# Kernel tuning notes

Measured on AMD Instinct MI355X. Metric: run time of the kernel, lower is better.

The kernel has to match this reference:

```python
import jax, jax.numpy as jnp
import numpy as np

B, C, H, W = 16, 256, 64, 64
DQ = C // 4


def setup_inputs() -> dict:
    key = jax.random.key(0)
    ks = jax.random.split(key, 6)
    scale = 1.0 / np.sqrt(C)
    return {
        "x_query": jax.random.normal(ks[0], (B, C, W, H), jnp.float32),
        "x_key": jax.random.normal(ks[1], (B, C, W, H), jnp.float32),
        "x_value": jax.random.normal(ks[2], (B, C, W, H), jnp.float32),
        "Wq": jax.random.normal(ks[3], (DQ, C), jnp.float32) * scale,
        "bq": jnp.zeros((DQ,), jnp.float32),
        "Wk": jax.random.normal(ks[4], (DQ, C), jnp.float32) * scale,
        "bk": jnp.zeros((DQ,), jnp.float32),
        "Wv": jax.random.normal(ks[5], (C, C), jnp.float32) * scale,
        "bv": jnp.zeros((C,), jnp.float32),
    }


def reference(x_query, x_key, x_value, Wq, bq, Wk, bk, Wv, bv):
    b, c, w, h = x_value.shape
    n = w * h
    # 1x1 convs == per-pixel linear over channels; flatten spatial to n
    q = (jnp.einsum('oc,bcn->bon', Wq, x_query.reshape(b, c, n))
         + bq[None, :, None])            # [b, dq, n]
    k = (jnp.einsum('oc,bcn->bon', Wk, x_key.reshape(b, c, n))
         + bk[None, :, None])            # [b, dq, n]
    v = (jnp.einsum('oc,bcn->bon', Wv, x_value.reshape(b, c, n))
         + bv[None, :, None])            # [b, c, n]
    # energy = Q^T K  (unscaled), softmax over last dim
    energy = jnp.einsum('bdi,bdj->bij', q, k)        # [b, n, n]
    attention = jax.nn.softmax(energy, axis=-1)
    # out = V @ attention : out[b,c,i] = sum_j V[b,c,j] * att[b,j,i]
    out = jnp.einsum('bcj,bji->bci', v, attention)   # [b, c, n]
    return out.reshape(b, c, w, h)
```

## Files before the change

### kernel.cpp

```cpp
#include <hip/hip_runtime.h>
#include <hip/hip_bf16.h>
#include <stddef.h>

#define BATCH 16
#define CH    256
#define NPIX  4096
#define DQH   64
#define L2E   1.44269504088896340736f

typedef __attribute__((ext_vector_type(8))) short bf16x8;
typedef __attribute__((ext_vector_type(4))) float floatx4;

__device__ __forceinline__ unsigned short f2bf(float f) {
  union { float f; unsigned int u; } v; v.f = f;
  unsigned int u = v.u;
  u += 0x7fffu + ((u >> 16) & 1u);
  return (unsigned short)(u >> 16);
}

__device__ __forceinline__ unsigned int pk2bf(float a, float b) {
  __hip_bfloat162 h = __float22bfloat162_rn(float2{a, b});
  union { __hip_bfloat162 h; unsigned int u; } cv;
  cv.h = h;
  return cv.u;
}

__device__ __forceinline__ bf16x8 ldbf8(const unsigned short* p) {
  return *(const bf16x8*)p;
}

__device__ __forceinline__ int xcd_swz(int lin, int nwg) {
  return (lin & 7) * (nwg >> 3) + (lin >> 3);
}

__device__ __forceinline__ void gload_lds16(const void* g, void* l) {
  __builtin_amdgcn_global_load_lds(
      (const __attribute__((address_space(1))) void*)g,
      (__attribute__((address_space(3))) void*)l, 16, 0, 0);
}

__global__ __launch_bounds__(256) void wconv_kernel(
    const float* __restrict__ Wq, const float* __restrict__ Wk,
    const float* __restrict__ Wv, unsigned short* __restrict__ Wb) {
  const int idx = blockIdx.x * 256 + threadIdx.x;
  float v;
  if (idx < 64 * CH)            v = Wq[idx] * L2E;
  else if (idx < 128 * CH)      v = Wk[idx - 64 * CH];
  else                          v = Wv[idx - 128 * CH];
  Wb[idx] = f2bf(v);
}

__global__ __launch_bounds__(256) void proj_kernel(
    const float* __restrict__ xq, const float* __restrict__ xk,
    const float* __restrict__ xv, const unsigned short* __restrict__ Wb,
    const float* __restrict__ bq, const float* __restrict__ bk,
    const float* __restrict__ bv,
    unsigned short* __restrict__ Qb, unsigned short* __restrict__ Kb,
    unsigned short* __restrict__ Vb) {
  __shared__ __attribute__((aligned(16))) float xtile[32][256];
  const int t    = threadIdx.x;
  const int lane = t & 63;
  const int w    = t >> 6;
  const int l15  = lane & 15;
  const int quad = lane >> 4;
  const int b    = blockIdx.y;
  const int pxbase = blockIdx.x * 256;
  const int z    = blockIdx.z;

  const float* X; const float* bt; int dbase; int wbase;
  if (z == 0)      { X = xq; bt = bq; dbase = 0;            wbase = 0; }
  else if (z == 1) { X = xk; bt = bk; dbase = 0;            wbase = 64; }
  else             { X = xv; bt = bv; dbase = (z - 2) * 64; wbase = 128 + (z - 2) * 64; }

  floatx4 acc[4][4];
#pragma unroll
  for (int mt = 0; mt < 4; ++mt)
#pragma unroll
    for (int nt = 0; nt < 4; ++nt)
      acc[mt][nt] = (floatx4){0.f, 0.f, 0.f, 0.f};

  const float* xb0 = X + (size_t)b * CH * NPIX + pxbase;

  for (int kb = 0; kb < 8; ++kb) {
#pragma unroll
    for (int i = 0; i < 8; ++i) {
      const int cloc = w + i * 4;
      const int rot  = (cloc >> 3) << 3;
      const int colf = ((lane << 2) - rot) & 255;
      gload_lds16(xb0 + (size_t)(kb * 32 + cloc) * NPIX + colf,
                  &xtile[cloc][0]);
    }
    __syncthreads();

#pragma unroll
    for (int nt = 0; nt < 4; ++nt) {
      const int pxl = w * 64 + nt * 16 + l15;
      float f[8];
#pragma unroll
      for (int j = 0; j < 8; ++j) {
        const int row = quad * 8 + j;
        f[j] = xtile[row][(pxl + ((row >> 3) << 3)) & 255];
      }
      union { bf16x8 v; unsigned int u[4]; } bb;
      bb.u[0] = pk2bf(f[0], f[1]);
      bb.u[1] = pk2bf(f[2], f[3]);
      bb.u[2] = pk2bf(f[4], f[5]);
      bb.u[3] = pk2bf(f[6], f[7]);
#pragma unroll
      for (int mt = 0; mt < 4; ++mt) {
        const bf16x8 aA =
            ldbf8(Wb + (size_t)(wbase + mt * 16 + l15) * CH + kb * 32 + quad * 8);
        acc[mt][nt] =
            __builtin_amdgcn_mfma_f32_16x16x32_bf16(aA, bb.v, acc[mt][nt], 0, 0, 0);
      }
    }
    __syncthreads();
  }

  float4 bias4[4];
#pragma unroll
  for (int mt = 0; mt < 4; ++mt)
    bias4[mt] = *(const float4*)&bt[dbase + mt * 16 + quad * 4];
  if (z == 0) {
#pragma unroll
    for (int mt = 0; mt < 4; ++mt) {
      bias4[mt].x *= L2E; bias4[mt].y *= L2E;
      bias4[mt].z *= L2E; bias4[mt].w *= L2E;
    }
  }

  if (z >= 2) {
#pragma unroll
    for (int mt = 0; mt < 4; ++mt)
#pragma unroll
      for (int nt = 0; nt < 4; ++nt) {
        const int px = pxbase + w * 64 + nt * 16 + l15;
#pragma unroll
        for (int r = 0; r < 4; ++r) {
          const int c = dbase + mt * 16 + quad * 4 + r;
          Vb[((size_t)b * CH + c) * NPIX + px] =
              f2bf(acc[mt][nt][r] + ((const float*)&bias4[mt])[r]);
        }
      }
  } else {
    unsigned short* Ob = (z == 0) ? Qb : Kb;
#pragma unroll
    for (int mt = 0; mt < 4; ++mt)
#pragma unroll
      for (int nt = 0; nt < 4; ++nt) {
        const int px = pxbase + w * 64 + nt * 16 + l15;
        uint2 qp;
        qp.x = pk2bf(acc[mt][nt][0] + ((const float*)&bias4[mt])[0],
                     acc[mt][nt][1] + ((const float*)&bias4[mt])[1]);
        qp.y = pk2bf(acc[mt][nt][2] + ((const float*)&bias4[mt])[2],
                     acc[mt][nt][3] + ((const float*)&bias4[mt])[3]);
        *(uint2*)&Ob[((size_t)b * NPIX + px) * DQH + mt * 16 + quad * 4] = qp;
      }
  }
}

__global__ __launch_bounds__(256) void pass1_kernel(
    const unsigned short* __restrict__ Qb, const unsigned short* __restrict__ Kb,
    float* __restrict__ Srow) {
  const int t    = threadIdx.x;
  const int lane = t & 63;
  const int w    = t >> 6;
  const int l15  = lane & 15;
  const int quad = lane >> 4;
  const int lin  = blockIdx.x + (blockIdx.y << 6);
  const int swz  = xcd_swz(lin, 64 * BATCH);
  const int b     = swz >> 6;
  const int jbase = (swz & 63) * 64 + w * 16;

  const unsigned short* qrow = Qb + ((size_t)b * NPIX + jbase + l15) * DQH;
  const bf16x8 qA0 = ldbf8(qrow + quad * 8);
  const bf16x8 qA1 = ldbf8(qrow + 32 + quad * 8);

  float lsum[4] = {0.f, 0.f, 0.f, 0.f};

  const unsigned short* kbase = Kb + (size_t)b * NPIX * DQH;

  bf16x8 kC[4][2], kN[4][2];
#pragma unroll
  for (int nt = 0; nt < 4; ++nt) {
    const unsigned short* krow = kbase + (size_t)(nt * 16 + l15) * DQH;
    kC[nt][0] = ldbf8(krow + quad * 8);
    kC[nt][1] = ldbf8(krow + 32 + quad * 8);
  }

  for (int ib = 0; ib < NPIX; ib += 64) {
    const int in = (ib + 64) & (NPIX - 1);
#pragma unroll
    for (int nt = 0; nt < 4; ++nt) {
      const unsigned short* krow = kbase + (size_t)(in + nt * 16 + l15) * DQH;
      kN[nt][0] = ldbf8(krow + quad * 8);
      kN[nt][1] = ldbf8(krow + 32 + quad * 8);
    }
#pragma unroll
    for (int nt = 0; nt < 4; ++nt) {
      floatx4 a = {0.f, 0.f, 0.f, 0.f};
      a = __builtin_amdgcn_mfma_f32_16x16x32_bf16(qA0, kC[nt][0], a, 0, 0, 0);
      a = __builtin_amdgcn_mfma_f32_16x16x32_bf16(qA1, kC[nt][1], a, 0, 0, 0);
#pragma unroll
      for (int r = 0; r < 4; ++r) lsum[r] += exp2f(a[r]);
    }
#pragma unroll
    for (int nt = 0; nt < 4; ++nt) {
      kC[nt][0] = kN[nt][0];
      kC[nt][1] = kN[nt][1];
    }
  }

#pragma unroll
  for (int r = 0; r < 4; ++r) {
    float s = lsum[r];
    s += __shfl_xor(s, 1);
    s += __shfl_xor(s, 2);
    s += __shfl_xor(s, 4);
    s += __shfl_xor(s, 8);
    if (l15 == 0)
      Srow[(size_t)b * NPIX + jbase + quad * 4 + r] = log2f(s);
  }
}

__global__ __launch_bounds__(256, 4) void pass2_kernel(
    const unsigned short* __restrict__ Qb, const unsigned short* __restrict__ Kb,
    const unsigned short* __restrict__ Vb, const float* __restrict__ Srow,
    float* __restrict__ out) {
  __shared__ __attribute__((aligned(16))) unsigned short Plds[2][64][72];
  __shared__ __attribute__((aligned(16))) unsigned short Qlds[2][64][72];
  const int t    = threadIdx.x;
  const int lane = t & 63;
  const int w    = t >> 6;
  const int l15  = lane & 15;
  const int quad = lane >> 4;
  const int lin  = blockIdx.x + (blockIdx.y << 6);
  const int swz  = xcd_swz(lin, 64 * BATCH);
  const int b     = swz >> 6;
  const int ibase = (swz & 63) * 64;

  const unsigned short* krow = Kb + ((size_t)b * NPIX + ibase + w * 16 + l15) * DQH;
  const bf16x8 kB0 = ldbf8(krow + quad * 8);
  const bf16x8 kB1 = ldbf8(krow + 32 + quad * 8);

  floatx4 accO[4][4];
#pragma unroll
  for (int mt = 0; mt < 4; ++mt)
#pragma unroll
    for (int nt = 0; nt < 4; ++nt)
      accO[mt][nt] = (floatx4){0.f, 0.f, 0.f, 0.f};

  const float* sp          = Srow + (size_t)b * NPIX;
  const unsigned short* qb = Qb + (size_t)b * NPIX * DQH;
  const unsigned short* vb = Vb + (size_t)b * CH * NPIX;

  const int srow = t >> 3;
  const int sseg = t & 7;

  {
    const unsigned short* qsrc = qb + (size_t)srow * DQH + sseg * 8;
    *(uint4*)&Qlds[0][srow][sseg * 8]      = *(const uint4*)qsrc;
    *(uint4*)&Qlds[0][srow + 32][sseg * 8] = *(const uint4*)(qsrc + 32 * DQH);
  }
  __syncthreads();

  int cur = 0;
  for (int jb = 0; jb < NPIX; jb += 64) {
    const int jn = (jb + 64) & (NPIX - 1);
    const unsigned short* qsrc = qb + (size_t)(jn + srow) * DQH + sseg * 8;
    const uint4 d0 = *(const uint4*)qsrc;
    const uint4 d1 = *(const uint4*)(qsrc + 32 * DQH);

#pragma unroll
    for (int jt = 0; jt < 4; ++jt) {
      const bf16x8 q0 = ldbf8(&Qlds[cur][jt * 16 + l15][quad * 8]);
      const bf16x8 q1 = ldbf8(&Qlds[cur][jt * 16 + l15][32 + quad * 8]);
      floatx4 a = {0.f, 0.f, 0.f, 0.f};
      a = __builtin_amdgcn_mfma_f32_16x16x32_bf16(q0, kB0, a, 0, 0, 0);
      a = __builtin_amdgcn_mfma_f32_16x16x32_bf16(q1, kB1, a, 0, 0, 0);
      const float4 s4 = *(const float4*)&sp[jb + jt * 16 + quad * 4];
      uint2 pk;
      pk.x = pk2bf(exp2f(a[0] - s4.x), exp2f(a[1] - s4.y));
      pk.y = pk2bf(exp2f(a[2] - s4.z), exp2f(a[3] - s4.w));
      *(uint2*)&Plds[cur][w * 16 + l15][jt * 16 + quad * 4] = pk;
    }

    *(uint4*)&Qlds[cur ^ 1][srow][sseg * 8]      = d0;
    *(uint4*)&Qlds[cur ^ 1][srow + 32][sseg * 8] = d1;

    __syncthreads();

#pragma unroll
    for (int ks = 0; ks < 2; ++ks) {
      bf16x8 pB[4];
#pragma unroll
      for (int nt = 0; nt < 4; ++nt)
        pB[nt] = ldbf8(&Plds[cur][nt * 16 + l15][ks * 32 + quad * 8]);
#pragma unroll
      for (int mt = 0; mt < 4; ++mt) {
        const unsigned short* vrow =
            vb + (size_t)(w * 64 + mt * 16 + l15) * NPIX + jb + ks * 32;
        const bf16x8 vA = ldbf8(vrow + quad * 8);
#pragma unroll
        for (int nt = 0; nt < 4; ++nt)
          accO[mt][nt] =
              __builtin_amdgcn_mfma_f32_16x16x32_bf16(vA, pB[nt], accO[mt][nt], 0, 0, 0);
      }
    }
    cur ^= 1;
  }

#pragma unroll
  for (int mt = 0; mt < 4; ++mt) {
#pragma unroll
    for (int nt = 0; nt < 4; ++nt) {
#pragma unroll
      for (int r = 0; r < 4; ++r) {
        const int c = w * 64 + mt * 16 + quad * 4 + r;
        const int i = ibase + nt * 16 + l15;
        out[((size_t)b * CH + c) * NPIX + i] = accO[mt][nt][r];
      }
    }
  }
}

extern "C" void kernel_launch(void* const* d_in, const int* in_sizes, int n_in,
                              void* d_out, int out_size, void* d_ws, size_t ws_size,
                              hipStream_t stream) {
  (void)in_sizes; (void)n_in; (void)out_size; (void)ws_size;
  const float* xq = (const float*)d_in[0];
  const float* xk = (const float*)d_in[1];
  const float* xv = (const float*)d_in[2];
  const float* Wq = (const float*)d_in[3];
  const float* bq = (const float*)d_in[4];
  const float* Wk = (const float*)d_in[5];
  const float* bk = (const float*)d_in[6];
  const float* Wv = (const float*)d_in[7];
  const float* bv = (const float*)d_in[8];
  float* out = (float*)d_out;

  char* ws = (char*)d_ws;
  const size_t qk_bytes = (size_t)BATCH * NPIX * DQH * 2;
  const size_t v_bytes  = (size_t)BATCH * CH * NPIX * 2;
  const size_t s_bytes  = (size_t)BATCH * NPIX * 4;
  unsigned short* Qb = (unsigned short*)(ws);
  unsigned short* Kb = (unsigned short*)(ws + qk_bytes);
  unsigned short* Vb = (unsigned short*)(ws + 2 * qk_bytes);
  float* Srow        = (float*)(ws + 2 * qk_bytes + v_bytes);
  unsigned short* Wb = (unsigned short*)(ws + 2 * qk_bytes + v_bytes + s_bytes);

  wconv_kernel<<<dim3(384), 256, 0, stream>>>(Wq, Wk, Wv, Wb);
  proj_kernel<<<dim3(16, 16, 6), 256, 0, stream>>>(xq, xk, xv, Wb, bq, bk, bv,
                                                   Qb, Kb, Vb);
  pass1_kernel<<<dim3(64, 16), 256, 0, stream>>>(Qb, Kb, Srow);
  pass2_kernel<<<dim3(64, 16), 256, 0, stream>>>(Qb, Kb, Vb, Srow, out);
}
```

Measured before the change: 755.8 us.

## Restructure pass2 into 32-row tiles with 8 waves, XOR-swizzled LDS and direct global-to-LDS loads

The pass2 tile shrinks from 64 to 32 query rows and grows from 4 to 8 waves per block. Each wave now computes one 16x16 piece of P and a 32-channel by 32-row piece of the output, and the grid doubles to 128x16 blocks. The double-buffered padded LDS arrays become single unpadded arrays with an XOR swizzle. Q tiles are fetched with gload_lds16 direct-to-LDS loads, which replaces the register-staged double buffering and adds a second barrier per iteration. The aim is more occupancy and parallelism with less LDS and fewer registers, at the cost of more recomputation of Q·K per output, more V reads per block, and a fully synchronous loop.

New measurement: 1.028 ms. 1.36x slower.

```diff
diff --git a/kernel.cpp b/kernel.cpp
--- a/kernel.cpp
+++ b/kernel.cpp
@@ -223,100 +223,98 @@
   }
 }
 
-__global__ __launch_bounds__(256, 4) void pass2_kernel(
+__global__ __launch_bounds__(512, 8) void pass2_kernel(
     const unsigned short* __restrict__ Qb, const unsigned short* __restrict__ Kb,
     const unsigned short* __restrict__ Vb, const float* __restrict__ Srow,
     float* __restrict__ out) {
-  __shared__ __attribute__((aligned(16))) unsigned short Plds[2][64][72];
-  __shared__ __attribute__((aligned(16))) unsigned short Qlds[2][64][72];
+  __shared__ __attribute__((aligned(16))) unsigned short Qlds[64][64];
+  __shared__ __attribute__((aligned(16))) unsigned short Plds[32][64];
   const int t    = threadIdx.x;
   const int lane = t & 63;
   const int w    = t >> 6;
   const int l15  = lane & 15;
   const int quad = lane >> 4;
-  const int lin  = blockIdx.x + (blockIdx.y << 6);
-  const int swz  = xcd_swz(lin, 64 * BATCH);
-  const int b     = swz >> 6;
-  const int ibase = (swz & 63) * 64;
-
-  const unsigned short* krow = Kb + ((size_t)b * NPIX + ibase + w * 16 + l15) * DQH;
+  const int lin  = blockIdx.x + (blockIdx.y << 7);
+  const int swz  = xcd_swz(lin, 128 * BATCH);
+  const int b     = swz >> 7;
+  const int ibase = (swz & 127) * 32;
+  const int is    = (w & 1) * 16;
+  const int js    = (w >> 1) * 16;
+  const int cb    = w * 32;
+
+  const unsigned short* krow = Kb + ((size_t)b * NPIX + ibase + is + l15) * DQH;
   const bf16x8 kB0 = ldbf8(krow + quad * 8);
   const bf16x8 kB1 = ldbf8(krow + 32 + quad * 8);
 
-  floatx4 accO[4][4];
-#pragma unroll
-  for (int mt = 0; mt < 4; ++mt)
-#pragma unroll
-    for (int nt = 0; nt < 4; ++nt)
+  floatx4 accO[2][2];
+#pragma unroll
+  for (int mt = 0; mt < 2; ++mt)
+#pragma unroll
+    for (int nt = 0; nt < 2; ++nt)
       accO[mt][nt] = (floatx4){0.f, 0.f, 0.f, 0.f};
 
   const float* sp          = Srow + (size_t)b * NPIX;
   const unsigned short* qb = Qb + (size_t)b * NPIX * DQH;
   const unsigned short* vb = Vb + (size_t)b * CH * NPIX;
 
-  const int srow = t >> 3;
-  const int sseg = t & 7;
-
-  {
-    const unsigned short* qsrc = qb + (size_t)srow * DQH + sseg * 8;
-    *(uint4*)&Qlds[0][srow][sseg * 8]      = *(const uint4*)qsrc;
-    *(uint4*)&Qlds[0][srow + 32][sseg * 8] = *(const uint4*)(qsrc + 32 * DQH);
-  }
+  const int qrw  = t >> 3;
+  const int qsof = (((t & 7) ^ (qrw & 7)) << 3);
+  unsigned short* qdst = &Qlds[(w & 7) * 8][0];
+
+  gload_lds16(qb + (size_t)qrw * DQH + qsof, qdst);
   __syncthreads();
 
-  int cur = 0;
   for (int jb = 0; jb < NPIX; jb += 64) {
+    const float4 s4 = *(const float4*)&sp[jb + js + quad * 4];
+    const int qr = js + l15;
+    const int qx = (qr & 7) << 4;
+    const bf16x8 q0 =
+        *(const bf16x8*)((const char*)&Qlds[qr][0] + ((quad * 16) ^ qx));
+    const bf16x8 q1 =
+        *(const bf16x8*)((const char*)&Qlds[qr][0] + ((64 + quad * 16) ^ qx));
+    floatx4 a = {0.f, 0.f, 0.f, 0.f};
+    a = __builtin_amdgcn_mfma_f32_16x16x32_bf16(q0, kB0, a, 0, 0, 0);
+    a = __builtin_amdgcn_mfma_f32_16x16x32_bf16(q1, kB1, a, 0, 0, 0);
+    uint2 pk;
+    pk.x = pk2bf(exp2f(a[0] - s4.x), exp2f(a[1] - s4.y));
+    pk.y = pk2bf(exp2f(a[2] - s4.z), exp2f(a[3] - s4.w));
+    const int pr = is + l15;
+    *(uint2*)((char*)&Plds[pr][0] +
+              ((js * 2 + quad * 8) ^ ((pr & 7) << 4))) = pk;
+    __syncthreads();
+
     const int jn = (jb + 64) & (NPIX - 1);
-    const unsigned short* qsrc = qb + (size_t)(jn + srow) * DQH + sseg * 8;
-    const uint4 d0 = *(const uint4*)qsrc;
-    const uint4 d1 = *(const uint4*)(qsrc + 32 * DQH);
-
-#pragma unroll
-    for (int jt = 0; jt < 4; ++jt) {
-      const bf16x8 q0 = ldbf8(&Qlds[cur][jt * 16 + l15][quad * 8]);
-      const bf16x8 q1 = ldbf8(&Qlds[cur][jt * 16 + l15][32 + quad * 8]);
-      floatx4 a = {0.f, 0.f, 0.f, 0.f};
-      a = __builtin_amdgcn_mfma_f32_16x16x32_bf16(q0, kB0, a, 0, 0, 0);
-      a = __builtin_amdgcn_mfma_f32_16x16x32_bf16(q1, kB1, a, 0, 0, 0);
-      const float4 s4 = *(const float4*)&sp[jb + jt * 16 + quad * 4];
-      uint2 pk;
-      pk.x = pk2bf(exp2f(a[0] - s4.x), exp2f(a[1] - s4.y));
-      pk.y = pk2bf(exp2f(a[2] - s4.z), exp2f(a[3] - s4.w));
-      *(uint2*)&Plds[cur][w * 16 + l15][jt * 16 + quad * 4] = pk;
-    }
-
-    *(uint4*)&Qlds[cur ^ 1][srow][sseg * 8]      = d0;
-    *(uint4*)&Qlds[cur ^ 1][srow + 32][sseg * 8] = d1;
-
+    gload_lds16(qb + (size_t)(jn + qrw) * DQH + qsof, qdst);
+
+#pragma unroll
+    for (int ks = 0; ks < 2; ++ks) {
+      bf16x8 pB[2];
+#pragma unroll
+      for (int nt = 0; nt < 2; ++nt) {
+        const int br = nt * 16 + l15;
+        pB[nt] = *(const bf16x8*)((const char*)&Plds[br][0] +
+                                  ((ks * 64 + quad * 16) ^ ((br & 7) << 4)));
+      }
+#pragma unroll
+      for (int mt = 0; mt < 2; ++mt) {
+        const bf16x8 vA = ldbf8(vb + (size_t)(cb + mt * 16 + l15) * NPIX +
+                                jb + ks * 32 + quad * 8);
+#pragma unroll
+        for (int nt = 0; nt < 2; ++nt)
+          accO[mt][nt] = __builtin_amdgcn_mfma_f32_16x16x32_bf16(
+              vA, pB[nt], accO[mt][nt], 0, 0, 0);
+      }
+    }
     __syncthreads();
-
-#pragma unroll
-    for (int ks = 0; ks < 2; ++ks) {
-      bf16x8 pB[4];
-#pragma unroll
-      for (int nt = 0; nt < 4; ++nt)
-        pB[nt] = ldbf8(&Plds[cur][nt * 16 + l15][ks * 32 + quad * 8]);
-#pragma unroll
-      for (int mt = 0; mt < 4; ++mt) {
-        const unsigned short* vrow =
-            vb + (size_t)(w * 64 + mt * 16 + l15) * NPIX + jb + ks * 32;
-        const bf16x8 vA = ldbf8(vrow + quad * 8);
-#pragma unroll
-        for (int nt = 0; nt < 4; ++nt)
-          accO[mt][nt] =
-              __builtin_amdgcn_mfma_f32_16x16x32_bf16(vA, pB[nt], accO[mt][nt], 0, 0, 0);
-      }
-    }
-    cur ^= 1;
-  }
-
-#pragma unroll
-  for (int mt = 0; mt < 4; ++mt) {
-#pragma unroll
-    for (int nt = 0; nt < 4; ++nt) {
+  }
+
+#pragma unroll
+  for (int mt = 0; mt < 2; ++mt) {
+#pragma unroll
+    for (int nt = 0; nt < 2; ++nt) {
 #pragma unroll
       for (int r = 0; r < 4; ++r) {
-        const int c = w * 64 + mt * 16 + quad * 4 + r;
+        const int c = cb + mt * 16 + quad * 4 + r;
         const int i = ibase + nt * 16 + l15;
         out[((size_t)b * CH + c) * NPIX + i] = accO[mt][nt][r];
       }
@@ -353,5 +351,5 @@
   proj_kernel<<<dim3(16, 16, 6), 256, 0, stream>>>(xq, xk, xv, Wb, bq, bk, bv,
                                                    Qb, Kb, Vb);
   pass1_kernel<<<dim3(64, 16), 256, 0, stream>>>(Qb, Kb, Srow);
-  pass2_kernel<<<dim3(64, 16), 256, 0, stream>>>(Qb, Kb, Vb, Srow, out);
-}
+  pass2_kernel<<<dim3(128, 16), 512, 0, stream>>>(Qb, Kb, Vb, Srow, out);
+}
```

## Stage V tiles in LDS via direct global-to-LDS loads with XOR-swizzled buffers

Applied to the files above, without the earlier changes.

Each wave now prefetches its 64 rows of the V tile into a shared Vlds buffer with direct global-to-LDS loads, issued after the MFMA step for the next j block. Previously every MFMA operand was a direct global load. The padded Q and P LDS arrays become unpadded with an XOR swizzle to avoid bank conflicts. The Srow loads are hoisted out of the inner loop, and the occupancy hint in launch_bounds is dropped. The cost is a larger LDS footprint, which lowers occupancy. The single-buffered V staging also depends on wait counts around the barrier for correctness.

Result: faster. 697.4 us (-7.7%).

```diff
diff --git a/kernel.cpp b/kernel.cpp
--- a/kernel.cpp
+++ b/kernel.cpp
@@ -223,12 +223,13 @@
   }
 }
 
-__global__ __launch_bounds__(256, 4) void pass2_kernel(
+__global__ __launch_bounds__(256) void pass2_kernel(
     const unsigned short* __restrict__ Qb, const unsigned short* __restrict__ Kb,
     const unsigned short* __restrict__ Vb, const float* __restrict__ Srow,
     float* __restrict__ out) {
-  __shared__ __attribute__((aligned(16))) unsigned short Plds[2][64][72];
-  __shared__ __attribute__((aligned(16))) unsigned short Qlds[2][64][72];
+  __shared__ __attribute__((aligned(16))) unsigned short Vlds[256][64];
+  __shared__ __attribute__((aligned(16))) unsigned short Qlds[2][64][64];
+  __shared__ __attribute__((aligned(16))) unsigned short Plds[2][64][64];
   const int t    = threadIdx.x;
   const int lane = t & 63;
   const int w    = t >> 6;
@@ -256,37 +257,56 @@
 
   const int srow = t >> 3;
   const int sseg = t & 7;
+  const int sswz = (sseg * 16) ^ ((srow & 7) << 4);
+
+  const int vrow0 = w * 64 + (lane >> 3);
+  const int vcol  = (((lane & 7) ^ (lane >> 3)) << 3);
 
   {
     const unsigned short* qsrc = qb + (size_t)srow * DQH + sseg * 8;
-    *(uint4*)&Qlds[0][srow][sseg * 8]      = *(const uint4*)qsrc;
-    *(uint4*)&Qlds[0][srow + 32][sseg * 8] = *(const uint4*)(qsrc + 32 * DQH);
-  }
+    *(uint4*)((char*)&Qlds[0][srow][0] + sswz)      = *(const uint4*)qsrc;
+    *(uint4*)((char*)&Qlds[0][srow + 32][0] + sswz) = *(const uint4*)(qsrc + 32 * DQH);
+  }
+#pragma unroll
+  for (int s = 0; s < 8; ++s)
+    gload_lds16(vb + (size_t)(vrow0 + s * 8) * NPIX + vcol,
+                &Vlds[w * 64 + s * 8][0]);
   __syncthreads();
 
   int cur = 0;
   for (int jb = 0; jb < NPIX; jb += 64) {
     const int jn = (jb + 64) & (NPIX - 1);
+
     const unsigned short* qsrc = qb + (size_t)(jn + srow) * DQH + sseg * 8;
     const uint4 d0 = *(const uint4*)qsrc;
     const uint4 d1 = *(const uint4*)(qsrc + 32 * DQH);
 
+    float4 s4[4];
+#pragma unroll
+    for (int jt = 0; jt < 4; ++jt)
+      s4[jt] = *(const float4*)&sp[jb + jt * 16 + quad * 4];
+
 #pragma unroll
     for (int jt = 0; jt < 4; ++jt) {
-      const bf16x8 q0 = ldbf8(&Qlds[cur][jt * 16 + l15][quad * 8]);
-      const bf16x8 q1 = ldbf8(&Qlds[cur][jt * 16 + l15][32 + quad * 8]);
+      const int qr = jt * 16 + l15;
+      const int qx = (qr & 7) << 4;
+      const bf16x8 q0 =
+          *(const bf16x8*)((const char*)&Qlds[cur][qr][0] + ((quad * 16) ^ qx));
+      const bf16x8 q1 =
+          *(const bf16x8*)((const char*)&Qlds[cur][qr][0] + ((64 + quad * 16) ^ qx));
       floatx4 a = {0.f, 0.f, 0.f, 0.f};
       a = __builtin_amdgcn_mfma_f32_16x16x32_bf16(q0, kB0, a, 0, 0, 0);
       a = __builtin_amdgcn_mfma_f32_16x16x32_bf16(q1, kB1, a, 0, 0, 0);
-      const float4 s4 = *(const float4*)&sp[jb + jt * 16 + quad * 4];
       uint2 pk;
-      pk.x = pk2bf(exp2f(a[0] - s4.x), exp2f(a[1] - s4.y));
-      pk.y = pk2bf(exp2f(a[2] - s4.z), exp2f(a[3] - s4.w));
-      *(uint2*)&Plds[cur][w * 16 + l15][jt * 16 + quad * 4] = pk;
-    }
-
-    *(uint4*)&Qlds[cur ^ 1][srow][sseg * 8]      = d0;
-    *(uint4*)&Qlds[cur ^ 1][srow + 32][sseg * 8] = d1;
+      pk.x = pk2bf(exp2f(a[0] - s4[jt].x), exp2f(a[1] - s4[jt].y));
+      pk.y = pk2bf(exp2f(a[2] - s4[jt].z), exp2f(a[3] - s4[jt].w));
+      const int pr = w * 16 + l15;
+      *(uint2*)((char*)&Plds[cur][pr][0] +
+                ((jt * 32 + quad * 8) ^ ((pr & 7) << 4))) = pk;
+    }
+
+    *(uint4*)((char*)&Qlds[cur ^ 1][srow][0] + sswz)      = d0;
+    *(uint4*)((char*)&Qlds[cur ^ 1][srow + 32][0] + sswz) = d1;
 
     __syncthreads();
 
@@ -294,19 +314,30 @@
     for (int ks = 0; ks < 2; ++ks) {
       bf16x8 pB[4];
 #pragma unroll
-      for (int nt = 0; nt < 4; ++nt)
-        pB[nt] = ldbf8(&Plds[cur][nt * 16 + l15][ks * 32 + quad * 8]);
+      for (int nt = 0; nt < 4; ++nt) {
+        const int br = nt * 16 + l15;
+        pB[nt] = *(const bf16x8*)((const char*)&Plds[cur][br][0] +
+                                  ((ks * 64 + quad * 16) ^ ((br & 7) << 4)));
+      }
 #pragma unroll
       for (int mt = 0; mt < 4; ++mt) {
-        const unsigned short* vrow =
-            vb + (size_t)(w * 64 + mt * 16 + l15) * NPIX + jb + ks * 32;
-        const bf16x8 vA = ldbf8(vrow + quad * 8);
+        const int vr = w * 64 + mt * 16 + l15;
+        const bf16x8 vA =
+            *(const bf16x8*)((const char*)&Vlds[vr][0] +
+                             ((ks * 64 + quad * 16) ^ ((l15 & 7) << 4)));
 #pragma unroll
         for (int nt = 0; nt < 4; ++nt)
-          accO[mt][nt] =
-              __builtin_amdgcn_mfma_f32_16x16x32_bf16(vA, pB[nt], accO[mt][nt], 0, 0, 0);
-      }
-    }
+          accO[mt][nt] = __builtin_amdgcn_mfma_f32_16x16x32_bf16(
+              vA, pB[nt], accO[mt][nt], 0, 0, 0);
+      }
+    }
+
+    __builtin_amdgcn_sched_barrier(0);
+#pragma unroll
+    for (int s = 0; s < 8; ++s)
+      gload_lds16(vb + (size_t)(vrow0 + s * 8) * NPIX + jn + vcol,
+                  &Vlds[w * 64 + s * 8][0]);
+
     cur ^= 1;
   }
 
```
